# Kernel optimization log

Measured on AMD Instinct MI355X. Metric: run time of the kernel, lower is better.

The kernel has to match this reference:

```python
import jax, jax.numpy as jnp
import numpy as np

N_NODES = 100_000
N_EDGES = 1_000_000
VOCAB = 131_075  # sym_vocab + 3
ES = 64
L = 2
DL = 256


def setup_inputs() -> dict:
    key = jax.random.key(0)
    ks = jax.random.split(key, 12)
    s = 0.05  # weight scale to keep activations bounded through scatter-add layers
    subj = jax.random.randint(ks[0], (N_EDGES,), 0, N_NODES, dtype=jnp.int32)
    pred = jax.random.randint(ks[1], (N_EDGES,), 0, VOCAB, dtype=jnp.int32)
    obj_rand = jax.random.randint(ks[2], (N_EDGES - N_NODES,), 0, N_NODES, dtype=jnp.int32)
    # guarantee every node appears as an obj so pooling over all N matches torch's node set
    obj = jnp.concatenate([jnp.arange(N_NODES, dtype=jnp.int32), obj_rand])
    return {
        "subj": subj,
        "pred": pred,
        "obj": obj,
        "sym_emb": jax.random.normal(ks[3], (VOCAB, ES), jnp.float32),
        "edge_emb": jax.random.normal(ks[4], (VOCAB, ES), jnp.float32),
        "msg_w1": jax.random.normal(ks[5], (L, 3 * ES, 2 * ES), jnp.float32) * s,
        "msg_b1": jax.random.normal(ks[6], (L, 2 * ES), jnp.float32) * s,
        "msg_w2": jax.random.normal(ks[7], (L, 2 * ES, ES), jnp.float32) * s,
        "msg_b2": jax.random.normal(ks[8], (L, ES), jnp.float32) * s,
        "to_latent_w": jax.random.normal(ks[9], (ES, DL), jnp.float32) * s,
        "to_latent_b": jax.random.normal(ks[10], (DL,), jnp.float32) * s,
        "n_nodes": N_NODES,
    }


def reference(subj, pred, obj, sym_emb, edge_emb, msg_w1, msg_b1, msg_w2, msg_b2,
              to_latent_w, to_latent_b, n_nodes):
    V = sym_emb.shape[0]
    # initial node states: embedding of node symbol id (id % vocab), node ids are 0..N-1
    h = sym_emb[jnp.arange(n_nodes) % V]                     # (N, es)
    e = edge_emb[pred % V]                                   # (E, es), same across layers
    for l in range(msg_w1.shape[0]):
        x = jnp.concatenate([h[subj], e, h[obj]], axis=-1)   # (E, 3*es) from OLD node states
        hmid = jax.nn.gelu(x @ msg_w1[l] + msg_b1[l], approximate=False)  # torch GELU = exact erf
        msg = hmid @ msg_w2[l] + msg_b2[l]                   # (E, es)
        h = h + jax.ops.segment_sum(msg, obj, num_segments=n_nodes)  # scatter-add to obj nodes
    pooled = h.mean(axis=0, keepdims=True)                   # (1, es)
    z_sym = pooled @ to_latent_w + to_latent_b               # (1, d_latent)
    return z_sym
```

## Files before the change

### kernel.cpp

```cpp
#include <hip/hip_runtime.h>
#include <hip/hip_bf16.h>


#define N_NODES 100000
#define NV_ELEMS (N_NODES * 64)
#define N_EDGES 1000000
#define EV_ELEMS (131075 * 64)
#define ES 64
#define TILE 32
#define NTILES (N_EDGES / TILE)
#define MSG_GRID 1024
#define SCAN_B 1024
#define SCAN_NB ((N_NODES + SCAN_B - 1) / SCAN_B)

typedef __bf16 bf16x8 __attribute__((ext_vector_type(8)));
typedef __bf16 bf16x4 __attribute__((ext_vector_type(4)));
typedef float f32x4 __attribute__((ext_vector_type(4)));

__device__ __forceinline__ f32x4 mfma_16x16x32(bf16x8 a, bf16x8 b, f32x4 c) {
    return __builtin_amdgcn_mfma_f32_16x16x32_bf16(a, b, c, 0, 0, 0);
}

#define BAR() asm volatile("s_waitcnt lgkmcnt(0)\n\ts_barrier" ::: "memory")

__device__ __forceinline__ f32x4 gelu4(f32x4 v) {
    f32x4 z = v * (v * v * -0.10294538f + -2.30227911f);
    f32x4 t;
#pragma unroll
    for (int i = 0; i < 4; ++i) t[i] = __builtin_amdgcn_exp2f(z[i]);
    f32x4 o = t + 1.0f;
    f32x4 r;
#pragma unroll
    for (int i = 0; i < 4; ++i) r[i] = __builtin_amdgcn_rcpf(o[i]);
    return v * r;
}

__global__ void k_init(const float* __restrict__ sym, const float* __restrict__ eemb,
                       const float* __restrict__ w1, const float* __restrict__ w2,
                       const int* __restrict__ obj,
                       float* __restrict__ A, __bf16* __restrict__ hb,
                       __bf16* __restrict__ ebb,
                       __bf16* __restrict__ w1b, __bf16* __restrict__ w2b,
                       float* __restrict__ pooled, int* __restrict__ cnt) {
    const int gid = blockIdx.x * blockDim.x + threadIdx.x;
    const int gstride = gridDim.x * blockDim.x;
    const int nv4 = NV_ELEMS / 4;
    const float4* s4 = (const float4*)sym;
    float4* a4 = (float4*)A;
    for (int i = gid; i < nv4; i += gstride) {
        float4 v = s4[i];
        a4[i] = v;
        bf16x4 p;
        p[0] = (__bf16)v.x; p[1] = (__bf16)v.y; p[2] = (__bf16)v.z; p[3] = (__bf16)v.w;
        *(bf16x4*)(hb + (size_t)i * 4) = p;
    }
    const int ev4 = EV_ELEMS / 4;
    const float4* e4 = (const float4*)eemb;
    for (int i = gid; i < ev4; i += gstride) {
        float4 v = e4[i];
        bf16x4 p;
        p[0] = (__bf16)v.x; p[1] = (__bf16)v.y; p[2] = (__bf16)v.z; p[3] = (__bf16)v.w;
        *(bf16x4*)(ebb + (size_t)i * 4) = p;
    }
    for (int d = gid; d < 2 * 24576; d += gstride) {
        int layer = d / 24576, r = d - layer * 24576;
        int kt = r >> 12, lg = (r >> 10) & 3, col = (r >> 3) & 127, i = r & 7;
        w1b[d] = (__bf16)w1[layer * 24576 + (kt * 32 + lg * 8 + i) * 128 + col];
    }
    for (int d = gid; d < 2 * 8192; d += gstride) {
        int layer = d >> 13, r = d & 8191;
        int kt = r >> 11, lg = (r >> 9) & 3, col = (r >> 3) & 63, i = r & 7;
        w2b[d] = (__bf16)w2[layer * 8192 + (kt * 32 + lg * 8 + i) * 64 + col];
    }
    for (int i = gid; i < N_EDGES; i += gstride) atomicAdd(&cnt[obj[i]], 1);
    if (gid < ES) pooled[gid] = 0.0f;
}

__global__ void k_h2b(const float* __restrict__ A, __bf16* __restrict__ hb) {
    const int nv4 = NV_ELEMS / 4;
    const float4* a4 = (const float4*)A;
    for (int i = blockIdx.x * blockDim.x + threadIdx.x; i < nv4;
         i += gridDim.x * blockDim.x) {
        float4 v = a4[i];
        bf16x4 p;
        p[0] = (__bf16)v.x; p[1] = (__bf16)v.y; p[2] = (__bf16)v.z; p[3] = (__bf16)v.w;
        *(bf16x4*)(hb + (size_t)i * 4) = p;
    }
}

__global__ __launch_bounds__(1024) void k_scanA(const int* __restrict__ cnt,
                                                int* __restrict__ off,
                                                int* __restrict__ bsum) {
    __shared__ int sp[SCAN_B];
    const int t = threadIdx.x;
    const int g = blockIdx.x * SCAN_B + t;
    int v = (g < N_NODES) ? cnt[g] : 0;
    sp[t] = v;
    __syncthreads();
#pragma unroll
    for (int d = 1; d < SCAN_B; d <<= 1) {
        int x = (t >= d) ? sp[t - d] : 0;
        __syncthreads();
        sp[t] += x;
        __syncthreads();
    }
    if (g < N_NODES) off[g] = sp[t] - v;
    if (t == SCAN_B - 1) bsum[blockIdx.x] = sp[t];
}

__global__ __launch_bounds__(1024) void k_scanC(int* __restrict__ off,
                                                const int* __restrict__ bsum,
                                                int* __restrict__ cur) {
    __shared__ int sboff;
    if (threadIdx.x == 0) {
        int run = 0;
        for (int b = 0; b < (int)blockIdx.x; ++b) run += bsum[b];
        sboff = run;
    }
    __syncthreads();
    const int g = blockIdx.x * SCAN_B + threadIdx.x;
    if (g < N_NODES) {
        int o = off[g] + sboff;
        off[g] = o;
        cur[g] = o;
    }
    if (g == 0) off[N_NODES] = N_EDGES;
}

__global__ void k_fill(const int* __restrict__ subj, const int* __restrict__ pred,
                       const int* __restrict__ obj, int* __restrict__ cur,
                       int4* __restrict__ eT) {
    int e0 = (blockIdx.x * blockDim.x + threadIdx.x) * 4;
    if (e0 >= N_EDGES) return;
    int4 s4 = *(const int4*)(subj + e0);
    int4 p4 = *(const int4*)(pred + e0);
    int4 o4 = *(const int4*)(obj + e0);
    int pos;
    pos = atomicAdd(&cur[o4.x], 1); eT[pos] = make_int4(s4.x, p4.x, o4.x, 0);
    pos = atomicAdd(&cur[o4.y], 1); eT[pos] = make_int4(s4.y, p4.y, o4.y, 0);
    pos = atomicAdd(&cur[o4.z], 1); eT[pos] = make_int4(s4.z, p4.z, o4.z, 0);
    pos = atomicAdd(&cur[o4.w], 1); eT[pos] = make_int4(s4.w, p4.w, o4.w, 0);
}

__global__ __launch_bounds__(256, 4) void k_msg(
    const int4* __restrict__ eT,
    const __bf16* __restrict__ hb, const __bf16* __restrict__ ebb,
    float* __restrict__ A,
    const __bf16* __restrict__ w1b, const float* __restrict__ b1,
    const __bf16* __restrict__ w2b, const float* __restrict__ b2) {
    __shared__ __bf16 sX[TILE][200];
    __shared__ __bf16 sHm[TILE][136];
    __shared__ float  sMsg[TILE][68];
    __shared__ int    sO2[2][TILE];

    const int tid = threadIdx.x;
    const int w   = tid >> 6;
    const int l   = tid & 63;
    const int lg  = l >> 4;
    const int lc  = l & 15;
    const int r  = tid >> 3;
    const int c8 = tid & 7;

    const __bf16* w1f = w1b + (size_t)(lg * 1024 + (w * 32 + lc) * 8);
    const __bf16* w2f = w2b + (size_t)(lg * 512 + (w * 16 + lc) * 8);
    bf16x8 wb1[6][2];
#pragma unroll
    for (int kt = 0; kt < 6; ++kt)
#pragma unroll
        for (int nt = 0; nt < 2; ++nt) {
            wb1[kt][nt] = *(const bf16x8*)(w1f + kt * 4096 + nt * 128);
            asm volatile("" : "+v"(wb1[kt][nt]));
        }
    bf16x8 wb2[4];
#pragma unroll
    for (int kt = 0; kt < 4; ++kt) {
        wb2[kt] = *(const bf16x8*)(w2f + kt * 2048);
        asm volatile("" : "+v"(wb2[kt]));
    }

    f32x4 b1q[2];
    b1q[0] = *(const f32x4*)(b1 + w * 32 + lg * 4);
    b1q[1] = *(const f32x4*)(b1 + w * 32 + 16 + lg * 4);
    f32x4 b2q = *(const f32x4*)(b2 + w * 16 + lg * 4);

    const int chunk = ((blockIdx.x & 7) << 7) + (blockIdx.x >> 3);
    int       tile  = (int)(((long long)chunk * NTILES) >> 10);
    const int tend  = (int)(((long long)(chunk + 1) * NTILES) >> 10);
    if (tile >= tend) return;

    int j0 = tile * TILE;
    int pp = 0;

    int4 ecur = eT[j0 + r];
    const int jn1 = (tile + 1 < tend) ? (tile + 1) * TILE : j0;
    int4 enxt = eT[jn1 + r];
    bf16x8 rb0 = *(const bf16x8*)(hb  + (size_t)ecur.x * ES + c8 * 8);
    bf16x8 rb1 = *(const bf16x8*)(ebb + (size_t)ecur.y * ES + c8 * 8);
    bf16x8 rb2 = *(const bf16x8*)(hb  + (size_t)ecur.z * ES + c8 * 8);

    for (; tile < tend; ++tile) {
        const int jf = (tile + 2 < tend) ? (tile + 2) * TILE : j0;

        *(bf16x8*)&sX[r][      c8 * 8] = rb0;
        *(bf16x8*)&sX[r][ 64 + c8 * 8] = rb1;
        *(bf16x8*)&sX[r][128 + c8 * 8] = rb2;
        if (c8 == 0) sO2[pp][r] = ecur.z;
        int4 efut = eT[jf + r];
        BAR();

        rb0 = *(const bf16x8*)(hb  + (size_t)enxt.x * ES + c8 * 8);
        rb1 = *(const bf16x8*)(ebb + (size_t)enxt.y * ES + c8 * 8);
        rb2 = *(const bf16x8*)(hb  + (size_t)enxt.z * ES + c8 * 8);

        f32x4 acc1[2][2];
#pragma unroll
        for (int nt = 0; nt < 2; ++nt)
#pragma unroll
            for (int mt = 0; mt < 2; ++mt) acc1[nt][mt] = (f32x4){0.f, 0.f, 0.f, 0.f};
#pragma unroll
        for (int kt = 0; kt < 6; ++kt) {
            bf16x8 x0 = *(const bf16x8*)&sX[lc][kt * 32 + lg * 8];
            bf16x8 x1 = *(const bf16x8*)&sX[16 + lc][kt * 32 + lg * 8];
            acc1[0][0] = mfma_16x16x32(wb1[kt][0], x0, acc1[0][0]);
            acc1[0][1] = mfma_16x16x32(wb1[kt][0], x1, acc1[0][1]);
            acc1[1][0] = mfma_16x16x32(wb1[kt][1], x0, acc1[1][0]);
            acc1[1][1] = mfma_16x16x32(wb1[kt][1], x1, acc1[1][1]);
        }

#pragma unroll
        for (int nt = 0; nt < 2; ++nt)
#pragma unroll
            for (int mt = 0; mt < 2; ++mt) {
                f32x4 g = gelu4(acc1[nt][mt] + b1q[nt]);
                bf16x4 hq;
#pragma unroll
                for (int rr = 0; rr < 4; ++rr) hq[rr] = (__bf16)g[rr];
                *(bf16x4*)&sHm[mt * 16 + lc][w * 32 + nt * 16 + lg * 4] = hq;
            }
        BAR();

        f32x4 acc2[2];
        acc2[0] = (f32x4){0.f, 0.f, 0.f, 0.f};
        acc2[1] = (f32x4){0.f, 0.f, 0.f, 0.f};
#pragma unroll
        for (int kt = 0; kt < 4; ++kt) {
            bf16x8 h0 = *(const bf16x8*)&sHm[lc][kt * 32 + lg * 8];
            bf16x8 h1 = *(const bf16x8*)&sHm[16 + lc][kt * 32 + lg * 8];
            acc2[0] = mfma_16x16x32(wb2[kt], h0, acc2[0]);
            acc2[1] = mfma_16x16x32(wb2[kt], h1, acc2[1]);
        }
        {
            f32x4 m0 = acc2[0] + b2q;
            f32x4 m1 = acc2[1] + b2q;
            *(f32x4*)&sMsg[lc][w * 16 + lg * 4]      = m0;
            *(f32x4*)&sMsg[16 + lc][w * 16 + lg * 4] = m1;
        }
        BAR();

        {
            const int c  = tid & 63;
            const int r0 = (tid >> 6) * 8;
            int   curo = sO2[pp][r0];
            float run  = sMsg[r0][c];
#pragma unroll
            for (int k2 = 1; k2 < 8; ++k2) {
                int   o = sO2[pp][r0 + k2];
                float v = sMsg[r0 + k2][c];
                if (o != curo) {
                    atomicAdd(&A[(size_t)curo * ES + c], run);
                    curo = o;
                    run  = v;
                } else {
                    run += v;
                }
            }
            atomicAdd(&A[(size_t)curo * ES + c], run);
        }
        ecur = enxt;
        enxt = efut;
        pp ^= 1;
    }
}

__global__ void k_pool(const float* __restrict__ h, float* __restrict__ pooled) {
    __shared__ float sm[256 * 4];
    const int nv4 = NV_ELEMS / 4;
    f32x4 acc = (f32x4){0.f, 0.f, 0.f, 0.f};
    for (int i4 = blockIdx.x * 256 + threadIdx.x; i4 < nv4; i4 += gridDim.x * 256)
        acc += *(const f32x4*)(h + (size_t)i4 * 4);
    *(f32x4*)&sm[threadIdx.x * 4] = acc;
    __syncthreads();
    if (threadIdx.x < 64) {
        const int q = threadIdx.x >> 2;
        const int j = threadIdx.x & 3;
        float s = 0.f;
#pragma unroll
        for (int m = 0; m < 16; ++m) s += sm[(m * 16 + q) * 4 + j];
        atomicAdd(&pooled[q * 4 + j], s);
    }
}

__global__ void k_final(const float* __restrict__ pooled, const float* __restrict__ w,
                        const float* __restrict__ b, float* __restrict__ out) {
    __shared__ float sp[64];
    if (threadIdx.x < 64) sp[threadIdx.x] = pooled[threadIdx.x] * (1.0f / N_NODES);
    __syncthreads();
    const int c = threadIdx.x;
    float s = b[c];
#pragma unroll
    for (int j = 0; j < 64; ++j) s += sp[j] * w[j * 256 + c];
    out[c] = s;
}

extern "C" void kernel_launch(void* const* d_in, const int* in_sizes, int n_in,
                              void* d_out, int out_size, void* d_ws, size_t ws_size,
                              hipStream_t stream) {
    const int*   subj = (const int*)d_in[0];
    const int*   pred = (const int*)d_in[1];
    const int*   obj  = (const int*)d_in[2];
    const float* sym  = (const float*)d_in[3];
    const float* eemb = (const float*)d_in[4];
    const float* w1   = (const float*)d_in[5];
    const float* b1   = (const float*)d_in[6];
    const float* w2   = (const float*)d_in[7];
    const float* b2   = (const float*)d_in[8];
    const float* lw   = (const float*)d_in[9];
    const float* lb   = (const float*)d_in[10];
    float* out = (float*)d_out;

    char* p = (char*)d_ws;
    float*  A      = (float*)p;   p += (size_t)NV_ELEMS * 4;
    __bf16* hb     = (__bf16*)p;  p += (size_t)NV_ELEMS * 2;
    __bf16* ebb    = (__bf16*)p;  p += (size_t)EV_ELEMS * 2;
    __bf16* w1b    = (__bf16*)p;  p += (size_t)2 * 24576 * 2;
    __bf16* w2b    = (__bf16*)p;  p += (size_t)2 * 8192 * 2;
    float*  pooled = (float*)p;   p += 256;
    int*    cnt    = (int*)p;     p += (size_t)N_NODES * 4;
    int*    off    = (int*)p;     p += (size_t)(N_NODES + 4) * 4;
    int*    cur    = (int*)p;     p += (size_t)N_NODES * 4;
    int4*   eT     = (int4*)p;    p += (size_t)N_EDGES * 16;
    int*    bsum   = (int*)p;     p += 400;
    int*    boff   = (int*)p;     p += 400;
    (void)ws_size;
    (void)boff;

    hipMemsetAsync(cnt, 0, (size_t)N_NODES * 4, stream);
    k_init<<<2048, 256, 0, stream>>>(sym, eemb, w1, w2, obj, A, hb, ebb, w1b, w2b,
                                     pooled, cnt);
    k_scanA<<<SCAN_NB, SCAN_B, 0, stream>>>(cnt, off, bsum);
    k_scanC<<<SCAN_NB, SCAN_B, 0, stream>>>(off, bsum, cur);
    k_fill<<<(N_EDGES / 4 + 255) / 256, 256, 0, stream>>>(subj, pred, obj, cur, eT);
    k_msg<<<MSG_GRID, 256, 0, stream>>>(eT, hb, ebb, A, w1b, b1, w2b, b2);
    k_h2b<<<2048, 256, 0, stream>>>(A, hb);
    k_msg<<<MSG_GRID, 256, 0, stream>>>(eT, hb, ebb, A, w1b + 24576, b1 + 128,
                                        w2b + 8192, b2 + 64);
    k_pool<<<256, 256, 0, stream>>>(A, pooled);
    k_final<<<1, 256, 0, stream>>>(pooled, lw, lb, out);
}
```

Baseline: 354.6 us.

## Double-buffer message tile and defer scatter reduction to next iteration

The message output buffer in shared memory becomes double-buffered. The segmented atomic reduction of tile t now runs after the first barrier of tile t+1, which removes one barrier per tile and lets the atomics overlap with the next tile's MFMA work. The gather loads for the next tile are also issued before the barrier instead of after it. The cost is extra shared memory and the risk of subtle ordering bugs between buffers.

```diff
diff --git a/kernel.cpp b/kernel.cpp
--- a/kernel.cpp
+++ b/kernel.cpp
@@ -150,7 +150,7 @@
     const __bf16* __restrict__ w2b, const float* __restrict__ b2) {
     __shared__ __bf16 sX[TILE][200];
     __shared__ __bf16 sHm[TILE][136];
-    __shared__ float  sMsg[TILE][68];
+    __shared__ float  sMsg[2][TILE][68];
     __shared__ int    sO2[2][TILE];
 
     const int tid = threadIdx.x;
@@ -183,6 +183,26 @@
     b1q[1] = *(const f32x4*)(b1 + w * 32 + 16 + lg * 4);
     f32x4 b2q = *(const f32x4*)(b2 + w * 16 + lg * 4);
 
+    const int rc  = tid & 63;
+    const int rr0 = (tid >> 6) * 8;
+#define REDUCE(BUF)                                                           \
+    do {                                                                      \
+        int   curo = sO2[BUF][rr0];                                           \
+        float run  = sMsg[BUF][rr0][rc];                                      \
+        _Pragma("unroll") for (int k2 = 1; k2 < 8; ++k2) {                    \
+            int   o = sO2[BUF][rr0 + k2];                                     \
+            float v = sMsg[BUF][rr0 + k2][rc];                                \
+            if (o != curo) {                                                  \
+                atomicAdd(&A[(size_t)curo * ES + rc], run);                   \
+                curo = o;                                                     \
+                run  = v;                                                     \
+            } else {                                                          \
+                run += v;                                                     \
+            }                                                                 \
+        }                                                                     \
+        atomicAdd(&A[(size_t)curo * ES + rc], run);                           \
+    } while (0)
+
     const int chunk = ((blockIdx.x & 7) << 7) + (blockIdx.x >> 3);
     int       tile  = (int)(((long long)chunk * NTILES) >> 10);
     const int tend  = (int)(((long long)(chunk + 1) * NTILES) >> 10);
@@ -190,6 +210,7 @@
 
     int j0 = tile * TILE;
     int pp = 0;
+    int havePrev = 0;
 
     int4 ecur = eT[j0 + r];
     const int jn1 = (tile + 1 < tend) ? (tile + 1) * TILE : j0;
@@ -205,12 +226,13 @@
         *(bf16x8*)&sX[r][ 64 + c8 * 8] = rb1;
         *(bf16x8*)&sX[r][128 + c8 * 8] = rb2;
         if (c8 == 0) sO2[pp][r] = ecur.z;
-        int4 efut = eT[jf + r];
-        BAR();
-
         rb0 = *(const bf16x8*)(hb  + (size_t)enxt.x * ES + c8 * 8);
         rb1 = *(const bf16x8*)(ebb + (size_t)enxt.y * ES + c8 * 8);
         rb2 = *(const bf16x8*)(hb  + (size_t)enxt.z * ES + c8 * 8);
+        int4 efut = eT[jf + r];
+        BAR();
+
+        if (havePrev) REDUCE(pp ^ 1);
 
         f32x4 acc1[2][2];
 #pragma unroll
@@ -252,34 +274,18 @@
         {
             f32x4 m0 = acc2[0] + b2q;
             f32x4 m1 = acc2[1] + b2q;
-            *(f32x4*)&sMsg[lc][w * 16 + lg * 4]      = m0;
-            *(f32x4*)&sMsg[16 + lc][w * 16 + lg * 4] = m1;
+            *(f32x4*)&sMsg[pp][lc][w * 16 + lg * 4]      = m0;
+            *(f32x4*)&sMsg[pp][16 + lc][w * 16 + lg * 4] = m1;
         }
-        BAR();
-
-        {
-            const int c  = tid & 63;
-            const int r0 = (tid >> 6) * 8;
-            int   curo = sO2[pp][r0];
-            float run  = sMsg[r0][c];
-#pragma unroll
-            for (int k2 = 1; k2 < 8; ++k2) {
-                int   o = sO2[pp][r0 + k2];
-                float v = sMsg[r0 + k2][c];
-                if (o != curo) {
-                    atomicAdd(&A[(size_t)curo * ES + c], run);
-                    curo = o;
-                    run  = v;
-                } else {
-                    run += v;
-                }
-            }
-            atomicAdd(&A[(size_t)curo * ES + c], run);
-        }
+
+        havePrev = 1;
         ecur = enxt;
         enxt = efut;
         pp ^= 1;
     }
+    BAR();
+    REDUCE(pp ^ 1);
+#undef REDUCE
 }
 
 __global__ void k_pool(const float* __restrict__ h, float* __restrict__ pooled) {
@@ -340,9 +346,7 @@
     int*    cur    = (int*)p;     p += (size_t)N_NODES * 4;
     int4*   eT     = (int4*)p;    p += (size_t)N_EDGES * 16;
     int*    bsum   = (int*)p;     p += 400;
-    int*    boff   = (int*)p;     p += 400;
     (void)ws_size;
-    (void)boff;
 
     hipMemsetAsync(cnt, 0, (size_t)N_NODES * 4, stream);
     k_init<<<2048, 256, 0, stream>>>(sym, eemb, w1, w2, obj, A, hb, ebb, w1b, w2b,
```

New measurement: 414.0 us. +16.8%, slower.

## Fuse both message layers and h-to-bf16 conversion into one persistent kernel

Applied to the files above, without the earlier changes.

Merges the two k_msg launches and the k_h2b conversion into a single persistent kernel (k_layers) that uses software grid barriers on a counter zeroed with the existing memset. The aim is to remove two kernel launch boundaries and their drain/ramp gaps. It is only used when the occupancy query reports at least 4 blocks per CU, so that all 1024 blocks can be co-resident. It adds the cost of spinning on global atomics and the risk of deadlock if residency assumptions fail.

```diff
diff --git a/kernel.cpp b/kernel.cpp
--- a/kernel.cpp
+++ b/kernel.cpp
@@ -33,6 +33,19 @@
 #pragma unroll
     for (int i = 0; i < 4; ++i) r[i] = __builtin_amdgcn_rcpf(o[i]);
     return v * r;
+}
+
+__device__ __forceinline__ void grid_barrier(int* ctr) {
+    __syncthreads();
+    __threadfence();
+    if (threadIdx.x == 0) {
+        __hip_atomic_fetch_add(ctr, 1, __ATOMIC_ACQ_REL, __HIP_MEMORY_SCOPE_AGENT);
+        while (__hip_atomic_load(ctr, __ATOMIC_ACQUIRE, __HIP_MEMORY_SCOPE_AGENT)
+               < (int)gridDim.x)
+            __builtin_amdgcn_s_sleep(8);
+    }
+    __syncthreads();
+    __threadfence();
 }
 
 __global__ void k_init(const float* __restrict__ sym, const float* __restrict__ eemb,
@@ -142,144 +155,180 @@
     pos = atomicAdd(&cur[o4.w], 1); eT[pos] = make_int4(s4.w, p4.w, o4.w, 0);
 }
 
+struct SmemT {
+    __bf16 sX[TILE][200];
+    __bf16 sHm[TILE][136];
+    float  sMsg[TILE][68];
+    int    sO2[2][TILE];
+};
+
+__device__ __forceinline__ void msg_layer(
+    SmemT& sm, const int4* __restrict__ eT,
+    const __bf16* __restrict__ hb, const __bf16* __restrict__ ebb,
+    float* __restrict__ A,
+    const __bf16* __restrict__ w1b, const float* __restrict__ b1,
+    const __bf16* __restrict__ w2b, const float* __restrict__ b2) {
+    const int tid = threadIdx.x;
+    const int w   = tid >> 6;
+    const int l   = tid & 63;
+    const int lg  = l >> 4;
+    const int lc  = l & 15;
+    const int r   = tid >> 3;
+    const int c8  = tid & 7;
+
+    const __bf16* w1f = w1b + (size_t)(lg * 1024 + (w * 32 + lc) * 8);
+    const __bf16* w2f = w2b + (size_t)(lg * 512 + (w * 16 + lc) * 8);
+    bf16x8 wb1[6][2];
+#pragma unroll
+    for (int kt = 0; kt < 6; ++kt)
+#pragma unroll
+        for (int nt = 0; nt < 2; ++nt) {
+            wb1[kt][nt] = *(const bf16x8*)(w1f + kt * 4096 + nt * 128);
+            asm volatile("" : "+v"(wb1[kt][nt]));
+        }
+    bf16x8 wb2[4];
+#pragma unroll
+    for (int kt = 0; kt < 4; ++kt) {
+        wb2[kt] = *(const bf16x8*)(w2f + kt * 2048);
+        asm volatile("" : "+v"(wb2[kt]));
+    }
+
+    f32x4 b1q[2];
+    b1q[0] = *(const f32x4*)(b1 + w * 32 + lg * 4);
+    b1q[1] = *(const f32x4*)(b1 + w * 32 + 16 + lg * 4);
+    f32x4 b2q = *(const f32x4*)(b2 + w * 16 + lg * 4);
+
+    const int chunk = ((blockIdx.x & 7) << 7) + (blockIdx.x >> 3);
+    int       tile  = (int)(((long long)chunk * NTILES) >> 10);
+    const int tend  = (int)(((long long)(chunk + 1) * NTILES) >> 10);
+    if (tile < tend) {
+        int j0 = tile * TILE;
+        int pp = 0;
+
+        int4 ecur = eT[j0 + r];
+        const int jn1 = (tile + 1 < tend) ? (tile + 1) * TILE : j0;
+        int4 enxt = eT[jn1 + r];
+        bf16x8 rb0 = *(const bf16x8*)(hb  + (size_t)ecur.x * ES + c8 * 8);
+        bf16x8 rb1 = *(const bf16x8*)(ebb + (size_t)ecur.y * ES + c8 * 8);
+        bf16x8 rb2 = *(const bf16x8*)(hb  + (size_t)ecur.z * ES + c8 * 8);
+
+        for (; tile < tend; ++tile) {
+            const int jf = (tile + 2 < tend) ? (tile + 2) * TILE : j0;
+
+            *(bf16x8*)&sm.sX[r][      c8 * 8] = rb0;
+            *(bf16x8*)&sm.sX[r][ 64 + c8 * 8] = rb1;
+            *(bf16x8*)&sm.sX[r][128 + c8 * 8] = rb2;
+            if (c8 == 0) sm.sO2[pp][r] = ecur.z;
+            int4 efut = eT[jf + r];
+            BAR();
+
+            rb0 = *(const bf16x8*)(hb  + (size_t)enxt.x * ES + c8 * 8);
+            rb1 = *(const bf16x8*)(ebb + (size_t)enxt.y * ES + c8 * 8);
+            rb2 = *(const bf16x8*)(hb  + (size_t)enxt.z * ES + c8 * 8);
+
+            f32x4 acc1[2][2];
+#pragma unroll
+            for (int nt = 0; nt < 2; ++nt)
+#pragma unroll
+                for (int mt = 0; mt < 2; ++mt) acc1[nt][mt] = (f32x4){0.f, 0.f, 0.f, 0.f};
+#pragma unroll
+            for (int kt = 0; kt < 6; ++kt) {
+                bf16x8 x0 = *(const bf16x8*)&sm.sX[lc][kt * 32 + lg * 8];
+                bf16x8 x1 = *(const bf16x8*)&sm.sX[16 + lc][kt * 32 + lg * 8];
+                acc1[0][0] = mfma_16x16x32(wb1[kt][0], x0, acc1[0][0]);
+                acc1[0][1] = mfma_16x16x32(wb1[kt][0], x1, acc1[0][1]);
+                acc1[1][0] = mfma_16x16x32(wb1[kt][1], x0, acc1[1][0]);
+                acc1[1][1] = mfma_16x16x32(wb1[kt][1], x1, acc1[1][1]);
+            }
+
+#pragma unroll
+            for (int nt = 0; nt < 2; ++nt)
+#pragma unroll
+                for (int mt = 0; mt < 2; ++mt) {
+                    f32x4 g = gelu4(acc1[nt][mt] + b1q[nt]);
+                    bf16x4 hq;
+#pragma unroll
+                    for (int rr = 0; rr < 4; ++rr) hq[rr] = (__bf16)g[rr];
+                    *(bf16x4*)&sm.sHm[mt * 16 + lc][w * 32 + nt * 16 + lg * 4] = hq;
+                }
+            BAR();
+
+            f32x4 acc2[2];
+            acc2[0] = (f32x4){0.f, 0.f, 0.f, 0.f};
+            acc2[1] = (f32x4){0.f, 0.f, 0.f, 0.f};
+#pragma unroll
+            for (int kt = 0; kt < 4; ++kt) {
+                bf16x8 h0 = *(const bf16x8*)&sm.sHm[lc][kt * 32 + lg * 8];
+                bf16x8 h1 = *(const bf16x8*)&sm.sHm[16 + lc][kt * 32 + lg * 8];
+                acc2[0] = mfma_16x16x32(wb2[kt], h0, acc2[0]);
+                acc2[1] = mfma_16x16x32(wb2[kt], h1, acc2[1]);
+            }
+            {
+                f32x4 m0 = acc2[0] + b2q;
+                f32x4 m1 = acc2[1] + b2q;
+                *(f32x4*)&sm.sMsg[lc][w * 16 + lg * 4]      = m0;
+                *(f32x4*)&sm.sMsg[16 + lc][w * 16 + lg * 4] = m1;
+            }
+            BAR();
+
+            {
+                const int c  = tid & 63;
+                const int r0 = (tid >> 6) * 8;
+                int   curo = sm.sO2[pp][r0];
+                float run  = sm.sMsg[r0][c];
+#pragma unroll
+                for (int k2 = 1; k2 < 8; ++k2) {
+                    int   o = sm.sO2[pp][r0 + k2];
+                    float v = sm.sMsg[r0 + k2][c];
+                    if (o != curo) {
+                        atomicAdd(&A[(size_t)curo * ES + c], run);
+                        curo = o;
+                        run  = v;
+                    } else {
+                        run += v;
+                    }
+                }
+                atomicAdd(&A[(size_t)curo * ES + c], run);
+            }
+            ecur = enxt;
+            enxt = efut;
+            pp ^= 1;
+        }
+    }
+}
+
 __global__ __launch_bounds__(256, 4) void k_msg(
     const int4* __restrict__ eT,
     const __bf16* __restrict__ hb, const __bf16* __restrict__ ebb,
     float* __restrict__ A,
     const __bf16* __restrict__ w1b, const float* __restrict__ b1,
     const __bf16* __restrict__ w2b, const float* __restrict__ b2) {
-    __shared__ __bf16 sX[TILE][200];
-    __shared__ __bf16 sHm[TILE][136];
-    __shared__ float  sMsg[TILE][68];
-    __shared__ int    sO2[2][TILE];
-
-    const int tid = threadIdx.x;
-    const int w   = tid >> 6;
-    const int l   = tid & 63;
-    const int lg  = l >> 4;
-    const int lc  = l & 15;
-    const int r  = tid >> 3;
-    const int c8 = tid & 7;
-
-    const __bf16* w1f = w1b + (size_t)(lg * 1024 + (w * 32 + lc) * 8);
-    const __bf16* w2f = w2b + (size_t)(lg * 512 + (w * 16 + lc) * 8);
-    bf16x8 wb1[6][2];
-#pragma unroll
-    for (int kt = 0; kt < 6; ++kt)
-#pragma unroll
-        for (int nt = 0; nt < 2; ++nt) {
-            wb1[kt][nt] = *(const bf16x8*)(w1f + kt * 4096 + nt * 128);
-            asm volatile("" : "+v"(wb1[kt][nt]));
+    __shared__ SmemT sm;
+    msg_layer(sm, eT, hb, ebb, A, w1b, b1, w2b, b2);
+}
+
+__global__ __launch_bounds__(256, 4) void k_layers(
+    const int4* __restrict__ eT, __bf16* __restrict__ hb,
+    const __bf16* __restrict__ ebb, float* __restrict__ A,
+    const __bf16* __restrict__ w1b, const float* __restrict__ b1,
+    const __bf16* __restrict__ w2b, const float* __restrict__ b2,
+    int* __restrict__ bctr) {
+    __shared__ SmemT sm;
+    msg_layer(sm, eT, hb, ebb, A, w1b, b1, w2b, b2);
+    grid_barrier(&bctr[0]);
+    {
+        const int nv4 = NV_ELEMS / 4;
+        const float4* a4 = (const float4*)A;
+        for (int i = blockIdx.x * 256 + threadIdx.x; i < nv4; i += MSG_GRID * 256) {
+            float4 v = a4[i];
+            bf16x4 p;
+            p[0] = (__bf16)v.x; p[1] = (__bf16)v.y;
+            p[2] = (__bf16)v.z; p[3] = (__bf16)v.w;
+            *(bf16x4*)(hb + (size_t)i * 4) = p;
         }
-    bf16x8 wb2[4];
-#pragma unroll
-    for (int kt = 0; kt < 4; ++kt) {
-        wb2[kt] = *(const bf16x8*)(w2f + kt * 2048);
-        asm volatile("" : "+v"(wb2[kt]));
-    }
-
-    f32x4 b1q[2];
-    b1q[0] = *(const f32x4*)(b1 + w * 32 + lg * 4);
-    b1q[1] = *(const f32x4*)(b1 + w * 32 + 16 + lg * 4);
-    f32x4 b2q = *(const f32x4*)(b2 + w * 16 + lg * 4);
-
-    const int chunk = ((blockIdx.x & 7) << 7) + (blockIdx.x >> 3);
-    int       tile  = (int)(((long long)chunk * NTILES) >> 10);
-    const int tend  = (int)(((long long)(chunk + 1) * NTILES) >> 10);
-    if (tile >= tend) return;
-
-    int j0 = tile * TILE;
-    int pp = 0;
-
-    int4 ecur = eT[j0 + r];
-    const int jn1 = (tile + 1 < tend) ? (tile + 1) * TILE : j0;
-    int4 enxt = eT[jn1 + r];
-    bf16x8 rb0 = *(const bf16x8*)(hb  + (size_t)ecur.x * ES + c8 * 8);
-    bf16x8 rb1 = *(const bf16x8*)(ebb + (size_t)ecur.y * ES + c8 * 8);
-    bf16x8 rb2 = *(const bf16x8*)(hb  + (size_t)ecur.z * ES + c8 * 8);
-
-    for (; tile < tend; ++tile) {
-        const int jf = (tile + 2 < tend) ? (tile + 2) * TILE : j0;
-
-        *(bf16x8*)&sX[r][      c8 * 8] = rb0;
-        *(bf16x8*)&sX[r][ 64 + c8 * 8] = rb1;
-        *(bf16x8*)&sX[r][128 + c8 * 8] = rb2;
-        if (c8 == 0) sO2[pp][r] = ecur.z;
-        int4 efut = eT[jf + r];
-        BAR();
-
-        rb0 = *(const bf16x8*)(hb  + (size_t)enxt.x * ES + c8 * 8);
-        rb1 = *(const bf16x8*)(ebb + (size_t)enxt.y * ES + c8 * 8);
-        rb2 = *(const bf16x8*)(hb  + (size_t)enxt.z * ES + c8 * 8);
-
-        f32x4 acc1[2][2];
-#pragma unroll
-        for (int nt = 0; nt < 2; ++nt)
-#pragma unroll
-            for (int mt = 0; mt < 2; ++mt) acc1[nt][mt] = (f32x4){0.f, 0.f, 0.f, 0.f};
-#pragma unroll
-        for (int kt = 0; kt < 6; ++kt) {
-            bf16x8 x0 = *(const bf16x8*)&sX[lc][kt * 32 + lg * 8];
-            bf16x8 x1 = *(const bf16x8*)&sX[16 + lc][kt * 32 + lg * 8];
-            acc1[0][0] = mfma_16x16x32(wb1[kt][0], x0, acc1[0][0]);
-            acc1[0][1] = mfma_16x16x32(wb1[kt][0], x1, acc1[0][1]);
-            acc1[1][0] = mfma_16x16x32(wb1[kt][1], x0, acc1[1][0]);
-            acc1[1][1] = mfma_16x16x32(wb1[kt][1], x1, acc1[1][1]);
-        }
-
-#pragma unroll
-        for (int nt = 0; nt < 2; ++nt)
-#pragma unroll
-            for (int mt = 0; mt < 2; ++mt) {
-                f32x4 g = gelu4(acc1[nt][mt] + b1q[nt]);
-                bf16x4 hq;
-#pragma unroll
-                for (int rr = 0; rr < 4; ++rr) hq[rr] = (__bf16)g[rr];
-                *(bf16x4*)&sHm[mt * 16 + lc][w * 32 + nt * 16 + lg * 4] = hq;
-            }
-        BAR();
-
-        f32x4 acc2[2];
-        acc2[0] = (f32x4){0.f, 0.f, 0.f, 0.f};
-        acc2[1] = (f32x4){0.f, 0.f, 0.f, 0.f};
-#pragma unroll
-        for (int kt = 0; kt < 4; ++kt) {
-            bf16x8 h0 = *(const bf16x8*)&sHm[lc][kt * 32 + lg * 8];
-            bf16x8 h1 = *(const bf16x8*)&sHm[16 + lc][kt * 32 + lg * 8];
-            acc2[0] = mfma_16x16x32(wb2[kt], h0, acc2[0]);
-            acc2[1] = mfma_16x16x32(wb2[kt], h1, acc2[1]);
-        }
-        {
-            f32x4 m0 = acc2[0] + b2q;
-            f32x4 m1 = acc2[1] + b2q;
-            *(f32x4*)&sMsg[lc][w * 16 + lg * 4]      = m0;
-            *(f32x4*)&sMsg[16 + lc][w * 16 + lg * 4] = m1;
-        }
-        BAR();
-
-        {
-            const int c  = tid & 63;
-            const int r0 = (tid >> 6) * 8;
-            int   curo = sO2[pp][r0];
-            float run  = sMsg[r0][c];
-#pragma unroll
-            for (int k2 = 1; k2 < 8; ++k2) {
-                int   o = sO2[pp][r0 + k2];
-                float v = sMsg[r0 + k2][c];
-                if (o != curo) {
-                    atomicAdd(&A[(size_t)curo * ES + c], run);
-                    curo = o;
-                    run  = v;
-                } else {
-                    run += v;
-                }
-            }
-            atomicAdd(&A[(size_t)curo * ES + c], run);
-        }
-        ecur = enxt;
-        enxt = efut;
-        pp ^= 1;
-    }
+    }
+    grid_barrier(&bctr[16]);
+    msg_layer(sm, eT, hb, ebb, A, w1b + 24576, b1 + 128, w2b + 8192, b2 + 64);
 }
 
 __global__ void k_pool(const float* __restrict__ h, float* __restrict__ pooled) {
@@ -336,24 +385,34 @@
     __bf16* w2b    = (__bf16*)p;  p += (size_t)2 * 8192 * 2;
     float*  pooled = (float*)p;   p += 256;
     int*    cnt    = (int*)p;     p += (size_t)N_NODES * 4;
+    int*    bctr   = (int*)p;     p += 128;
     int*    off    = (int*)p;     p += (size_t)(N_NODES + 4) * 4;
     int*    cur    = (int*)p;     p += (size_t)N_NODES * 4;
     int4*   eT     = (int4*)p;    p += (size_t)N_EDGES * 16;
     int*    bsum   = (int*)p;     p += 400;
-    int*    boff   = (int*)p;     p += 400;
     (void)ws_size;
-    (void)boff;
-
-    hipMemsetAsync(cnt, 0, (size_t)N_NODES * 4, stream);
+
+    int maxb = 0;
+    hipError_t qerr = hipOccupancyMaxActiveBlocksPerMultiprocessor(&maxb, k_layers,
+                                                                   256, 0);
+    const bool fused = (qerr == hipSuccess && maxb >= 4);
+
+    hipMemsetAsync(cnt, 0, (size_t)N_NODES * 4 + 128, stream);
     k_init<<<2048, 256, 0, stream>>>(sym, eemb, w1, w2, obj, A, hb, ebb, w1b, w2b,
                                      pooled, cnt);
     k_scanA<<<SCAN_NB, SCAN_B, 0, stream>>>(cnt, off, bsum);
     k_scanC<<<SCAN_NB, SCAN_B, 0, stream>>>(off, bsum, cur);
     k_fill<<<(N_EDGES / 4 + 255) / 256, 256, 0, stream>>>(subj, pred, obj, cur, eT);
-    k_msg<<<MSG_GRID, 256, 0, stream>>>(eT, hb, ebb, A, w1b, b1, w2b, b2);
-    k_h2b<<<2048, 256, 0, stream>>>(A, hb);
-    k_msg<<<MSG_GRID, 256, 0, stream>>>(eT, hb, ebb, A, w1b + 24576, b1 + 128,
-                                        w2b + 8192, b2 + 64);
+
+    if (fused) {
+        k_layers<<<MSG_GRID, 256, 0, stream>>>(eT, hb, ebb, A, w1b, b1, w2b, b2,
+                                               bctr);
+    } else {
+        k_msg<<<MSG_GRID, 256, 0, stream>>>(eT, hb, ebb, A, w1b, b1, w2b, b2);
+        k_h2b<<<2048, 256, 0, stream>>>(A, hb);
+        k_msg<<<MSG_GRID, 256, 0, stream>>>(eT, hb, ebb, A, w1b + 24576, b1 + 128,
+                                            w2b + 8192, b2 + 64);
+    }
     k_pool<<<256, 256, 0, stream>>>(A, pooled);
     k_final<<<1, 256, 0, stream>>>(pooled, lw, lb, out);
 }
```

After: 554.3 us. +56.3%, slower.
